# Performance work log

Measured on AMD Instinct MI355X. Metric: run time of the kernel, lower is better.

Reference implementation:

```python
import jax, jax.numpy as jnp
import numpy as np

WINDOW_SIZE = 11
SIGMA = 1.5
C1 = 0.01 ** 2
C2 = 0.03 ** 2


def _gaussian_1d(window_size, sigma):
    x = np.arange(window_size, dtype=np.float32)
    g = np.exp(-((x - window_size // 2) ** 2) / (2.0 * sigma ** 2))
    g = g / g.sum()
    return jnp.asarray(g, dtype=jnp.float32)


def _blur(x, g1d):
    # Separable depthwise Gaussian blur, SAME padding.
    # x: [B, C, H, W]; mathematically identical to conv with outer(g, g).
    c = x.shape[1]
    pad = WINDOW_SIZE // 2
    kh = jnp.broadcast_to(g1d.reshape(1, 1, WINDOW_SIZE, 1), (c, 1, WINDOW_SIZE, 1))
    kw = jnp.broadcast_to(g1d.reshape(1, 1, 1, WINDOW_SIZE), (c, 1, 1, WINDOW_SIZE))
    dn = ('NCHW', 'OIHW', 'NCHW')
    x = jax.lax.conv_general_dilated(x, kh, (1, 1), [(pad, pad), (0, 0)],
                                     dimension_numbers=dn, feature_group_count=c)
    x = jax.lax.conv_general_dilated(x, kw, (1, 1), [(0, 0), (pad, pad)],
                                     dimension_numbers=dn, feature_group_count=c)
    return x


def setup_inputs() -> dict:
    key = jax.random.key(0)
    k1, k2 = jax.random.split(key)
    shape = (32, 1, 512, 512)
    img1 = jax.random.uniform(k1, shape, dtype=jnp.float32)
    img2 = jax.random.uniform(k2, shape, dtype=jnp.float32)
    return {"img1": img1, "img2": img2}


def reference(img1, img2):
    g1d = _gaussian_1d(WINDOW_SIZE, SIGMA)
    mu1 = _blur(img1, g1d)
    mu2 = _blur(img2, g1d)
    mu1_sq = mu1 * mu1
    mu2_sq = mu2 * mu2
    mu1_mu2 = mu1 * mu2
    sigma1_sq = _blur(img1 * img1, g1d) - mu1_sq
    sigma2_sq = _blur(img2 * img2, g1d) - mu2_sq
    sigma12 = _blur(img1 * img2, g1d) - mu1_mu2
    ssim_map = ((2.0 * mu1_mu2 + C1) * (2.0 * sigma12 + C2)) / (
        (mu1_sq + mu2_sq + C1) * (sigma1_sq + sigma2_sq + C2))
    return ssim_map.mean()  # size_average=True
```

## Files before the change

kernel.cpp:

```cpp
#include <hip/hip_runtime.h>

#define HH 512
#define WW 512
#define BATCH 32
#define BH 16
#define NB (HH / BH)
#define TPB 256
#define VTW 528
#define NBLOCKS (NB * BATCH)
#define CBASE 0xAAAAAAAAu


__global__ __launch_bounds__(TPB, 4) void ssim_main(
    const float* __restrict__ img1,
    const float* __restrict__ img2,
    unsigned* __restrict__ counter,
    float* __restrict__ partial,
    float* __restrict__ out)
{
  constexpr float G[11] = {
      0.00102838f, 0.00759876f, 0.03600077f, 0.10936070f, 0.21300553f,
      0.26601171f,
      0.21300553f, 0.10936070f, 0.03600077f, 0.00759876f, 0.00102838f};
  constexpr float C1 = 1.0e-4f;
  constexpr float C2 = 9.0e-4f;

  const int tid  = threadIdx.x;
  const int band = blockIdx.x;
  const int bat  = blockIdx.y;
  const int r0   = band * BH;
  const float* p1 = img1 + (size_t)bat * (HH * WW);
  const float* p2 = img2 + (size_t)bat * (HH * WW);
  const int c0 = tid * 2;
  const int rr = tid >> 7;
  const int cg = tid & 127;

  __shared__ __align__(16) float pb[2][5][VTW];
  __shared__ float  wsum[4];
  __shared__ double dsum[4];
  __shared__ int    amlast;

  if (tid < 16) {
    const int p = tid >> 3, o = tid & 7;
#pragma unroll
    for (int a = 0; a < 5; ++a) {
      pb[p][a][o]       = 0.f;
      pb[p][a][520 + o] = 0.f;
    }
  }

  float2 w1[12], w2[12];
#pragma unroll
  for (int j = 0; j < 12; ++j) {
    const int r = r0 - 5 + j;
    float2 a = make_float2(0.f, 0.f), b = a;
    if (r >= 0 && r < HH) {
      a = *(const float2*)(p1 + r * WW + c0);
      b = *(const float2*)(p2 + r * WW + c0);
    }
    w1[j] = a; w2[j] = b;
  }

  __syncthreads();

  float ssum = 0.f;

#pragma unroll 1
  for (int q = 0; q < BH; q += 2) {
    float2 ta1 = make_float2(0.f, 0.f), ta2 = ta1, tb1 = ta1, tb2 = ta1;
    if (q + 2 < BH) {
      const int ra = r0 + 7 + q;
      const int rb = r0 + 8 + q;
      if (ra < HH) {
        ta1 = *(const float2*)(p1 + ra * WW + c0);
        ta2 = *(const float2*)(p2 + ra * WW + c0);
      }
      if (rb < HH) {
        tb1 = *(const float2*)(p1 + rb * WW + c0);
        tb2 = *(const float2*)(p2 + rb * WW + c0);
      }
    }

    float acc[2][5][2];
#pragma unroll
    for (int r = 0; r < 2; ++r)
#pragma unroll
      for (int a = 0; a < 5; ++a) { acc[r][a][0] = 0.f; acc[r][a][1] = 0.f; }

#pragma unroll
    for (int j = 0; j < 12; ++j) {
      const float2 xa = w1[j];
      const float2 ya = w2[j];
      const float xv[2] = {xa.x, xa.y};
      const float yv[2] = {ya.x, ya.y};
#pragma unroll
      for (int i = 0; i < 2; ++i) {
        const float x  = xv[i], y = yv[i];
        const float xx = x * x, yy = y * y, xy = x * y;
        if (j < 11) {
          const float gk = G[j];
          acc[0][0][i] = fmaf(gk, x,  acc[0][0][i]);
          acc[0][1][i] = fmaf(gk, y,  acc[0][1][i]);
          acc[0][2][i] = fmaf(gk, xx, acc[0][2][i]);
          acc[0][3][i] = fmaf(gk, yy, acc[0][3][i]);
          acc[0][4][i] = fmaf(gk, xy, acc[0][4][i]);
        }
        if (j >= 1) {
          const float gk = G[j - 1];
          acc[1][0][i] = fmaf(gk, x,  acc[1][0][i]);
          acc[1][1][i] = fmaf(gk, y,  acc[1][1][i]);
          acc[1][2][i] = fmaf(gk, xx, acc[1][2][i]);
          acc[1][3][i] = fmaf(gk, yy, acc[1][3][i]);
          acc[1][4][i] = fmaf(gk, xy, acc[1][4][i]);
        }
      }
    }

#pragma unroll
    for (int r = 0; r < 2; ++r)
#pragma unroll
      for (int a = 0; a < 5; ++a)
        ((float2*)(&pb[r][a][0]))[4 + tid] =
            make_float2(acc[r][a][0], acc[r][a][1]);

    __syncthreads();

    float h[5][4];
#pragma unroll
    for (int a = 0; a < 5; ++a) {
      const float4* r4 = (const float4*)(&pb[rr][a][0]);
      const float4 X0 = r4[cg];
      const float4 X1 = r4[cg + 1];
      const float4 X2 = r4[cg + 2];
      const float4 X3 = r4[cg + 3];
      const float4 X4 = r4[cg + 4];
      const float x[20] = {X0.x, X0.y, X0.z, X0.w, X1.x, X1.y, X1.z, X1.w,
                           X2.x, X2.y, X2.z, X2.w, X3.x, X3.y, X3.z, X3.w,
                           X4.x, X4.y, X4.z, X4.w};
#pragma unroll
      for (int j = 0; j < 4; ++j) {
        float hv = 0.f;
#pragma unroll
        for (int k = 0; k < 11; ++k) hv = fmaf(G[k], x[j + 3 + k], hv);
        h[a][j] = hv;
      }
    }

#pragma unroll
    for (int j = 0; j < 4; ++j) {
      const float mu1 = h[0][j], mu2 = h[1][j];
      const float mu12 = mu1 * mu2;
      const float mu1s = mu1 * mu1;
      const float mu2s = mu2 * mu2;
      const float sg1  = h[2][j] - mu1s;
      const float sg2  = h[3][j] - mu2s;
      const float sg12 = h[4][j] - mu12;
      const float num = (2.f * mu12 + C1) * (2.f * sg12 + C2);
      const float den = (mu1s + mu2s + C1) * (sg1 + sg2 + C2);
      float rn = __builtin_amdgcn_rcpf(den);
      rn = rn * fmaf(-den, rn, 2.0f);
      ssum = fmaf(num, rn, ssum);
    }

    __syncthreads();

#pragma unroll
    for (int j = 0; j < 10; ++j) { w1[j] = w1[j + 2]; w2[j] = w2[j + 2]; }
    w1[10] = ta1; w2[10] = ta2;
    w1[11] = tb1; w2[11] = tb2;
  }

#pragma unroll
  for (int off = 32; off > 0; off >>= 1) ssum += __shfl_xor(ssum, off, 64);
  if ((tid & 63) == 0) wsum[tid >> 6] = ssum;
  __syncthreads();
  if (tid == 0) {
    const float bsum = wsum[0] + wsum[1] + wsum[2] + wsum[3];
    atomicExch(&partial[bat * NB + band], bsum);
    __threadfence();
    const unsigned old = atomicAdd(counter, 1u);
    amlast = (old == CBASE + (unsigned)NBLOCKS - 1u) ? 1 : 0;
  }
  __syncthreads();
  if (amlast) {
    double s = 0.0;
    for (int i = tid; i < NBLOCKS; i += TPB)
      s += (double)atomicAdd(&partial[i], 0.0f);
#pragma unroll
    for (int off = 32; off > 0; off >>= 1) s += __shfl_xor(s, off, 64);
    if ((tid & 63) == 0) dsum[tid >> 6] = s;
    __syncthreads();
    if (tid == 0)
      out[0] = (float)((dsum[0] + dsum[1] + dsum[2] + dsum[3]) /
                       (double)((size_t)BATCH * HH * WW));
  }
}

extern "C" void kernel_launch(void* const* d_in, const int* in_sizes, int n_in,
                              void* d_out, int out_size, void* d_ws, size_t ws_size,
                              hipStream_t stream) {
  const float* img1 = (const float*)d_in[0];
  const float* img2 = (const float*)d_in[1];
  float* out = (float*)d_out;
  unsigned* counter = (unsigned*)d_ws;
  float* partial = (float*)((char*)d_ws + 16);
  dim3 grid(NB, BATCH);
  ssim_main<<<grid, TPB, 0, stream>>>(img1, img2, counter, partial, out);
}
```

Measured before the change: 130.3 us.

## Process four rows per iteration with one wave per row and swizzled LDS

The vertical pass now produces four output rows per loop iteration from a 14-row register window instead of two rows from 12, which halves the number of barriers per row. In the horizontal pass each wave now owns one full row and each lane computes 8 outputs from 18 loaded values, instead of 4 from 20. The halo padding columns are replaced by lane-edge zeroing plus an XOR-swizzled shared-memory layout meant to avoid bank conflicts. The cost is more live registers and twice the shared memory per block (40 KB), which may limit occupancy or cause spills.

```diff
diff --git a/kernel.cpp b/kernel.cpp
--- a/kernel.cpp
+++ b/kernel.cpp
@@ -6,7 +6,6 @@
 #define BH 16
 #define NB (HH / BH)
 #define TPB 256
-#define VTW 528
 #define NBLOCKS (NB * BATCH)
 #define CBASE 0xAAAAAAAAu
 
@@ -26,32 +25,37 @@
   constexpr float C2 = 9.0e-4f;
 
   const int tid  = threadIdx.x;
+  const int L    = tid & 63;
+  const int rr   = tid >> 6;
   const int band = blockIdx.x;
   const int bat  = blockIdx.y;
   const int r0   = band * BH;
   const float* p1 = img1 + (size_t)bat * (HH * WW);
   const float* p2 = img2 + (size_t)bat * (HH * WW);
   const int c0 = tid * 2;
-  const int rr = tid >> 7;
-  const int cg = tid & 127;
-
-  __shared__ __align__(16) float pb[2][5][VTW];
-  __shared__ float  wsum[4];
-  __shared__ double dsum[4];
-  __shared__ int    amlast;
-
-  if (tid < 16) {
-    const int p = tid >> 3, o = tid & 7;
-#pragma unroll
-    for (int a = 0; a < 5; ++a) {
-      pb[p][a][o]       = 0.f;
-      pb[p][a][520 + o] = 0.f;
-    }
-  }
-
-  float2 w1[12], w2[12];
-#pragma unroll
-  for (int j = 0; j < 12; ++j) {
+
+  __shared__ __align__(16) float4 pbuf4[4 * 5 * 128];
+  float* sp = (float*)pbuf4;
+
+  const int wu4  = tid >> 1;
+  const int wOff = ((wu4 ^ ((wu4 >> 3) & 1)) << 2) + ((tid & 1) << 1);
+
+  const int uLo = (2 * L - 2 < 0) ? 0 : 2 * L - 2;
+  const int u0  = (2 * L - 1 < 0) ? 0 : 2 * L - 1;
+  const int u1  = 2 * L;
+  const int u2  = 2 * L + 1;
+  const int u3  = (2 * L + 2 > 127) ? 127 : 2 * L + 2;
+  const int uHi = (2 * L + 3 > 127) ? 127 : 2 * L + 3;
+  const int sLo = ((uLo ^ ((uLo >> 3) & 1)) << 2) + 3;
+  const int s0  = (u0 ^ ((u0 >> 3) & 1)) << 2;
+  const int s1  = (u1 ^ ((u1 >> 3) & 1)) << 2;
+  const int s2  = (u2 ^ ((u2 >> 3) & 1)) << 2;
+  const int s3  = (u3 ^ ((u3 >> 3) & 1)) << 2;
+  const int sHi = (uHi ^ ((uHi >> 3) & 1)) << 2;
+
+  float2 w1[14], w2[14];
+#pragma unroll
+  for (int j = 0; j < 14; ++j) {
     const int r = r0 - 5 + j;
     float2 a = make_float2(0.f, 0.f), b = a;
     if (r >= 0 && r < HH) {
@@ -61,93 +65,96 @@
     w1[j] = a; w2[j] = b;
   }
 
-  __syncthreads();
-
   float ssum = 0.f;
 
 #pragma unroll 1
-  for (int q = 0; q < BH; q += 2) {
-    float2 ta1 = make_float2(0.f, 0.f), ta2 = ta1, tb1 = ta1, tb2 = ta1;
-    if (q + 2 < BH) {
-      const int ra = r0 + 7 + q;
-      const int rb = r0 + 8 + q;
-      if (ra < HH) {
-        ta1 = *(const float2*)(p1 + ra * WW + c0);
-        ta2 = *(const float2*)(p2 + ra * WW + c0);
+  for (int q = 0; q < BH; q += 4) {
+    float2 t1[4], t2[4];
+#pragma unroll
+    for (int j = 0; j < 4; ++j) { t1[j] = make_float2(0.f, 0.f); t2[j] = t1[j]; }
+    if (q + 4 < BH) {
+#pragma unroll
+      for (int j = 0; j < 4; ++j) {
+        const int r = r0 + q + 9 + j;
+        if (r < HH) {
+          t1[j] = *(const float2*)(p1 + r * WW + c0);
+          t2[j] = *(const float2*)(p2 + r * WW + c0);
+        }
       }
-      if (rb < HH) {
-        tb1 = *(const float2*)(p1 + rb * WW + c0);
-        tb2 = *(const float2*)(p2 + rb * WW + c0);
-      }
-    }
-
-    float acc[2][5][2];
-#pragma unroll
-    for (int r = 0; r < 2; ++r)
+    }
+
+    float acc[4][5][2];
+#pragma unroll
+    for (int r = 0; r < 4; ++r)
 #pragma unroll
       for (int a = 0; a < 5; ++a) { acc[r][a][0] = 0.f; acc[r][a][1] = 0.f; }
 
 #pragma unroll
-    for (int j = 0; j < 12; ++j) {
-      const float2 xa = w1[j];
-      const float2 ya = w2[j];
+    for (int e = 0; e < 14; ++e) {
+      const float2 xa = w1[e];
+      const float2 ya = w2[e];
       const float xv[2] = {xa.x, xa.y};
       const float yv[2] = {ya.x, ya.y};
 #pragma unroll
       for (int i = 0; i < 2; ++i) {
         const float x  = xv[i], y = yv[i];
         const float xx = x * x, yy = y * y, xy = x * y;
-        if (j < 11) {
-          const float gk = G[j];
-          acc[0][0][i] = fmaf(gk, x,  acc[0][0][i]);
-          acc[0][1][i] = fmaf(gk, y,  acc[0][1][i]);
-          acc[0][2][i] = fmaf(gk, xx, acc[0][2][i]);
-          acc[0][3][i] = fmaf(gk, yy, acc[0][3][i]);
-          acc[0][4][i] = fmaf(gk, xy, acc[0][4][i]);
-        }
-        if (j >= 1) {
-          const float gk = G[j - 1];
-          acc[1][0][i] = fmaf(gk, x,  acc[1][0][i]);
-          acc[1][1][i] = fmaf(gk, y,  acc[1][1][i]);
-          acc[1][2][i] = fmaf(gk, xx, acc[1][2][i]);
-          acc[1][3][i] = fmaf(gk, yy, acc[1][3][i]);
-          acc[1][4][i] = fmaf(gk, xy, acc[1][4][i]);
+#pragma unroll
+        for (int r = 0; r < 4; ++r) {
+          if (e >= r && e <= r + 10) {
+            const float g = G[e - r];
+            acc[r][0][i] = fmaf(g, x,  acc[r][0][i]);
+            acc[r][1][i] = fmaf(g, y,  acc[r][1][i]);
+            acc[r][2][i] = fmaf(g, xx, acc[r][2][i]);
+            acc[r][3][i] = fmaf(g, yy, acc[r][3][i]);
+            acc[r][4][i] = fmaf(g, xy, acc[r][4][i]);
+          }
         }
       }
     }
 
 #pragma unroll
-    for (int r = 0; r < 2; ++r)
+    for (int r = 0; r < 4; ++r)
 #pragma unroll
       for (int a = 0; a < 5; ++a)
-        ((float2*)(&pb[r][a][0]))[4 + tid] =
+        *(float2*)(sp + ((r * 5 + a) << 9) + wOff) =
             make_float2(acc[r][a][0], acc[r][a][1]);
 
+#pragma unroll
+    for (int j = 0; j < 10; ++j) { w1[j] = w1[j + 4]; w2[j] = w2[j + 4]; }
+#pragma unroll
+    for (int j = 0; j < 4; ++j) { w1[10 + j] = t1[j]; w2[10 + j] = t2[j]; }
+
     __syncthreads();
 
-    float h[5][4];
+    float h[5][8];
 #pragma unroll
     for (int a = 0; a < 5; ++a) {
-      const float4* r4 = (const float4*)(&pb[rr][a][0]);
-      const float4 X0 = r4[cg];
-      const float4 X1 = r4[cg + 1];
-      const float4 X2 = r4[cg + 2];
-      const float4 X3 = r4[cg + 3];
-      const float4 X4 = r4[cg + 4];
-      const float x[20] = {X0.x, X0.y, X0.z, X0.w, X1.x, X1.y, X1.z, X1.w,
-                           X2.x, X2.y, X2.z, X2.w, X3.x, X3.y, X3.z, X3.w,
-                           X4.x, X4.y, X4.z, X4.w};
-#pragma unroll
-      for (int j = 0; j < 4; ++j) {
+      const int base = (rr * 5 + a) << 9;
+      float x[18];
+      x[0] = sp[base + sLo];
+      const float4 X0 = *(const float4*)(sp + base + s0);
+      const float4 X1 = *(const float4*)(sp + base + s1);
+      const float4 X2 = *(const float4*)(sp + base + s2);
+      const float4 X3 = *(const float4*)(sp + base + s3);
+      x[17] = sp[base + sHi];
+      x[1] = X0.x;  x[2] = X0.y;  x[3] = X0.z;  x[4] = X0.w;
+      x[5] = X1.x;  x[6] = X1.y;  x[7] = X1.z;  x[8] = X1.w;
+      x[9] = X2.x;  x[10] = X2.y; x[11] = X2.z; x[12] = X2.w;
+      x[13] = X3.x; x[14] = X3.y; x[15] = X3.z; x[16] = X3.w;
+      if (L == 0)  { x[0] = x[1] = x[2] = x[3] = x[4] = 0.f; }
+      if (L == 63) { x[13] = x[14] = x[15] = x[16] = x[17] = 0.f; }
+#pragma unroll
+      for (int j = 0; j < 8; ++j) {
         float hv = 0.f;
 #pragma unroll
-        for (int k = 0; k < 11; ++k) hv = fmaf(G[k], x[j + 3 + k], hv);
+        for (int k = 0; k < 11; ++k) hv = fmaf(G[k], x[j + k], hv);
         h[a][j] = hv;
       }
     }
 
 #pragma unroll
-    for (int j = 0; j < 4; ++j) {
+    for (int j = 0; j < 8; ++j) {
       const float mu1 = h[0][j], mu2 = h[1][j];
       const float mu12 = mu1 * mu2;
       const float mu1s = mu1 * mu1;
@@ -163,35 +170,33 @@
     }
 
     __syncthreads();
-
-#pragma unroll
-    for (int j = 0; j < 10; ++j) { w1[j] = w1[j + 2]; w2[j] = w2[j + 2]; }
-    w1[10] = ta1; w2[10] = ta2;
-    w1[11] = tb1; w2[11] = tb2;
   }
 
 #pragma unroll
   for (int off = 32; off > 0; off >>= 1) ssum += __shfl_xor(ssum, off, 64);
-  if ((tid & 63) == 0) wsum[tid >> 6] = ssum;
+  float*  wred = sp;
+  double* dred = (double*)(sp + 8);
+  int*    flag = (int*)(sp + 16);
+  if (L == 0) wred[rr] = ssum;
   __syncthreads();
   if (tid == 0) {
-    const float bsum = wsum[0] + wsum[1] + wsum[2] + wsum[3];
+    const float bsum = wred[0] + wred[1] + wred[2] + wred[3];
     atomicExch(&partial[bat * NB + band], bsum);
     __threadfence();
     const unsigned old = atomicAdd(counter, 1u);
-    amlast = (old == CBASE + (unsigned)NBLOCKS - 1u) ? 1 : 0;
+    flag[0] = (old == CBASE + (unsigned)NBLOCKS - 1u) ? 1 : 0;
   }
   __syncthreads();
-  if (amlast) {
+  if (flag[0]) {
     double s = 0.0;
     for (int i = tid; i < NBLOCKS; i += TPB)
       s += (double)atomicAdd(&partial[i], 0.0f);
 #pragma unroll
     for (int off = 32; off > 0; off >>= 1) s += __shfl_xor(s, off, 64);
-    if ((tid & 63) == 0) dsum[tid >> 6] = s;
+    if (L == 0) dred[rr] = s;
     __syncthreads();
     if (tid == 0)
-      out[0] = (float)((dsum[0] + dsum[1] + dsum[2] + dsum[3]) /
+      out[0] = (float)((dred[0] + dred[1] + dred[2] + dred[3]) /
                        (double)((size_t)BATCH * HH * WW));
   }
 }
```

New measurement: 191.8 us. 47.2% more time.
